# Kernel tuning notes

Measured on AMD Instinct MI355X. Metric: run time of the kernel, lower is better.

The kernel has to match this reference:

```python
import jax, jax.numpy as jnp
import numpy as np

LRELU_SLOPE = 0.2
FUSED_SCALE = float(np.sqrt(2.0))


def _haar_kernels():
    l = np.ones((1, 2), np.float32) / np.sqrt(np.float32(2.0))
    h = l.copy()
    h[0, 0] = -h[0, 0]
    ll = l.T @ l
    lh = h.T @ l
    hl = l.T @ h
    hh = h.T @ h
    return jnp.asarray(ll), jnp.asarray(lh), jnp.asarray(hl), jnp.asarray(hh)


def _blur_kernel():
    k = np.array([1.0, 3.0, 3.0, 1.0], np.float32)
    k = np.outer(k, k)
    k = k / k.sum()
    return jnp.asarray(k)


def upfirdn2d(x, k, up=1, down=1, pad=(0, 0)):
    """Faithful upfirdn2d: zero-upsample by `up`, pad, FIR filter (true
    convolution, i.e. flipped kernel), then stride-`down` decimation.
    Implemented as a single lax conv with lhs_dilation; the extra (up-1)
    trailing pad reproduces torch's H*up zero-padded upsampling."""
    if len(pad) == 2:
        px0, px1, py0, py1 = pad[0], pad[1], pad[0], pad[1]
    else:
        px0, px1, py0, py1 = pad
    B, C, H, W = x.shape
    w = jnp.flip(k, (0, 1))[None, None].astype(x.dtype)  # [1,1,kh,kw]
    out = jax.lax.conv_general_dilated(
        x.reshape(B * C, 1, H, W), w,
        window_strides=(down, down),
        padding=((py0, py1 + up - 1), (px0, px1 + up - 1)),
        lhs_dilation=(up, up),
        dimension_numbers=('NCHW', 'OIHW', 'NCHW'))
    return out.reshape(B, C, out.shape[2], out.shape[3])


def setup_inputs() -> dict:
    key = jax.random.key(0)
    k1, k2 = jax.random.split(key)
    B, C_wt, H, W = 32, 12, 256, 256
    out_channel = 256
    x = jax.random.normal(k1, (B, C_wt, H, W), dtype=jnp.float32)
    weight = jax.random.normal(k2, (out_channel, C_wt, 1, 1), dtype=jnp.float32)
    bias = jnp.zeros((out_channel,), dtype=jnp.float32)
    return {"x": x, "weight": weight, "bias": bias}


def reference(x, weight, bias):
    ll, lh, hl, hh = _haar_kernels()
    c = x.shape[1] // 4
    # InverseHaarTransform (iwt kernels: ll, -lh, -hl, hh), up=2, pad=(1,0,1,0)
    parts = (x[:, 0*c:1*c], x[:, 1*c:2*c], x[:, 2*c:3*c], x[:, 3*c:4*c])
    kerns = (ll, -lh, -hl, hh)
    y = upfirdn2d(parts[0], kerns[0], up=2, pad=(1, 0, 1, 0))
    for p, kk in zip(parts[1:], kerns[1:]):
        y = y + upfirdn2d(p, kk, up=2, pad=(1, 0, 1, 0))
    # Downsample: blur kernel [1,3,3,1], factor=2 -> pad=(1,1), down=2
    y = upfirdn2d(y, _blur_kernel(), down=2, pad=(1, 1))
    # HaarTransform: down=2, pad=(0,0)
    t = jnp.concatenate([upfirdn2d(y, kk, down=2) for kk in (ll, lh, hl, hh)], axis=1)
    # EqualConv2d 1x1 (scale = 1/sqrt(in_channel*k^2), no conv bias) + FusedLeakyReLU
    scale = 1.0 / np.sqrt(np.float32(weight.shape[1]))  # kernel_size = 1
    out = jnp.einsum('bchw,oc->bohw', t, weight[:, :, 0, 0] * scale)
    out = jax.nn.leaky_relu(out + bias[None, :, None, None], LRELU_SLOPE) * FUSED_SCALE
    return t, out
```

## Files before the change

kernel.cpp:

```cpp
#include <hip/hip_runtime.h>


#define T_ELEMS 6291456
#define HW_T    16384
#define HW_X    65536

typedef float f4v __attribute__((ext_vector_type(4)));

__global__ __launch_bounds__(256) void wavelet_t_kernel(
    const float* __restrict__ x, float* __restrict__ t)
{
    const int tid = threadIdx.x;
    const int q   = tid & 31;
    const int ur  = tid >> 5;
    const int u   = blockIdx.x * 8 + ur;
    const int ch  = blockIdx.y;
    const int b   = blockIdx.z;

    const float F[2][2][4] = {
        { { 1.f,  7.f,  7.f,  1.f}, {-1.f, -1.f, 1.f,  1.f} },
        { { 1.f,  5.f, -5.f, -1.f}, {-1.f,  1.f, 1.f, -1.f} }
    };

    float acc[4][4];
    #pragma unroll
    for (int k = 0; k < 4; ++k)
        #pragma unroll
        for (int p = 0; p < 4; ++p) acc[k][p] = 0.f;

    const int r0    = 2 * u - 1;
    const int cbase = 8 * q;

    #pragma unroll
    for (int g = 0; g < 4; ++g) {
        const int gr = g & 1, gc = g >> 1;
        const float* xp = x + ((size_t)(b * 12 + g * 3 + ch)) * HW_X;
        #pragma unroll
        for (int dy = 0; dy < 4; ++dy) {
            const int r = r0 + dy;
            float c[10];
            if (r >= 0 && r < 256) {
                const float* rp = xp + (r << 8) + cbase;
                const float4 A = *reinterpret_cast<const float4*>(rp);
                const float4 B = *reinterpret_cast<const float4*>(rp + 4);
                c[1] = A.x; c[2] = A.y; c[3] = A.z; c[4] = A.w;
                c[5] = B.x; c[6] = B.y; c[7] = B.z; c[8] = B.w;
                float left = 0.f, right = 0.f;
                if (q > 0)  left  = rp[-1];
                if (q < 31) right = rp[8];
                c[0] = left; c[9] = right;
            } else {
                #pragma unroll
                for (int i = 0; i < 10; ++i) c[i] = 0.f;
            }
            #pragma unroll
            for (int p = 0; p < 4; ++p) {
                float s0 = 0.f, s1 = 0.f;
                #pragma unroll
                for (int dx = 0; dx < 4; ++dx) {
                    s0 = fmaf(F[0][gc][dx], c[2 * p + dx], s0);
                    s1 = fmaf(F[1][gc][dx], c[2 * p + dx], s1);
                }
                acc[0][p] = fmaf(F[0][gr][dy], s0, acc[0][p]);
                acc[1][p] = fmaf(F[1][gr][dy], s0, acc[1][p]);
                acc[2][p] = fmaf(F[0][gr][dy], s1, acc[2][p]);
                acc[3][p] = fmaf(F[1][gr][dy], s1, acc[3][p]);
            }
        }
    }

    const float sc = 1.f / 256.f;
    #pragma unroll
    for (int k = 0; k < 4; ++k) {
        float4 o;
        o.x = acc[k][0] * sc; o.y = acc[k][1] * sc;
        o.z = acc[k][2] * sc; o.w = acc[k][3] * sc;
        *reinterpret_cast<float4*>(
            t + ((size_t)(b * 12 + k * 3 + ch)) * HW_T + (u << 7) + 4 * q) = o;
    }
}

__global__ __launch_bounds__(256) void conv1x1_kernel(
    const float* __restrict__ t, const float* __restrict__ w,
    const float* __restrict__ bias, float* __restrict__ out)
{
    __shared__ float ws[128 * 12];
    __shared__ float bs[128];
    const int tid = threadIdx.x;
    const int b   = blockIdx.y;
    const int oz  = blockIdx.z;

    const float scale = 0.2886751345948129f;
    for (int i = tid; i < 1536; i += 256) ws[i] = w[oz * 1536 + i] * scale;
    if (tid < 128) bs[tid] = bias[oz * 128 + tid];
    __syncthreads();

    const int base = blockIdx.x * 1024 + tid * 4;

    float4 tv[12];
    #pragma unroll
    for (int c = 0; c < 12; ++c)
        tv[c] = *reinterpret_cast<const float4*>(t + ((size_t)(b * 12 + c)) * HW_T + base);

    const float SQ2 = 1.4142135623730951f;
    float* outp = out + ((size_t)(b * 256 + oz * 128)) * HW_T + base;

    #pragma unroll 4
    for (int oo = 0; oo < 128; ++oo) {
        const float4 w0 = *reinterpret_cast<const float4*>(&ws[oo * 12 + 0]);
        const float4 w1 = *reinterpret_cast<const float4*>(&ws[oo * 12 + 4]);
        const float4 w2 = *reinterpret_cast<const float4*>(&ws[oo * 12 + 8]);
        const float bo = bs[oo];
        float4 a = make_float4(bo, bo, bo, bo);
        #pragma unroll
        for (int c = 0; c < 4; ++c) {
            const float wv = (&w0.x)[c];
            a.x = fmaf(tv[c].x, wv, a.x); a.y = fmaf(tv[c].y, wv, a.y);
            a.z = fmaf(tv[c].z, wv, a.z); a.w = fmaf(tv[c].w, wv, a.w);
        }
        #pragma unroll
        for (int c = 0; c < 4; ++c) {
            const float wv = (&w1.x)[c];
            a.x = fmaf(tv[c + 4].x, wv, a.x); a.y = fmaf(tv[c + 4].y, wv, a.y);
            a.z = fmaf(tv[c + 4].z, wv, a.z); a.w = fmaf(tv[c + 4].w, wv, a.w);
        }
        #pragma unroll
        for (int c = 0; c < 4; ++c) {
            const float wv = (&w2.x)[c];
            a.x = fmaf(tv[c + 8].x, wv, a.x); a.y = fmaf(tv[c + 8].y, wv, a.y);
            a.z = fmaf(tv[c + 8].z, wv, a.z); a.w = fmaf(tv[c + 8].w, wv, a.w);
        }
        a.x = fmaxf(a.x, 0.2f * a.x) * SQ2;
        a.y = fmaxf(a.y, 0.2f * a.y) * SQ2;
        a.z = fmaxf(a.z, 0.2f * a.z) * SQ2;
        a.w = fmaxf(a.w, 0.2f * a.w) * SQ2;

        f4v av = { a.x, a.y, a.z, a.w };
        __builtin_nontemporal_store(
            av, reinterpret_cast<f4v*>(outp + (size_t)oo * HW_T));
    }
}

extern "C" void kernel_launch(void* const* d_in, const int* in_sizes, int n_in,
                              void* d_out, int out_size, void* d_ws, size_t ws_size,
                              hipStream_t stream) {
    const float* x    = (const float*)d_in[0];
    const float* wgt  = (const float*)d_in[1];
    const float* bias = (const float*)d_in[2];
    float* t   = (float*)d_out;
    float* out = t + T_ELEMS;

    dim3 b1(256, 1, 1), g1(16, 3, 32);
    hipLaunchKernelGGL(wavelet_t_kernel, g1, b1, 0, stream, x, t);

    dim3 b2(256, 1, 1), g2(16, 32, 2);
    hipLaunchKernelGGL(conv1x1_kernel, g2, b2, 0, stream, t, wgt, bias, out);
}
```

Baseline: 153.3 us.

## Fuse wavelet transform and 1x1 conv into a single kernel

```diff
diff --git a/kernel.cpp b/kernel.cpp
--- a/kernel.cpp
+++ b/kernel.cpp
@@ -7,135 +7,131 @@
 
 typedef float f4v __attribute__((ext_vector_type(4)));
 
-__global__ __launch_bounds__(256) void wavelet_t_kernel(
-    const float* __restrict__ x, float* __restrict__ t)
+__global__ __launch_bounds__(256) void fused_fromrgb_kernel(
+    const float* __restrict__ x, const float* __restrict__ w,
+    const float* __restrict__ bias, float* __restrict__ t,
+    float* __restrict__ out)
 {
+    __shared__ float ws[256 * 12];
+    __shared__ float bs[256];
     const int tid = threadIdx.x;
+
+    const float wscale = 0.2886751345948129f;
+    bs[tid] = bias[tid];
+    #pragma unroll
+    for (int i = 0; i < 12; ++i)
+        ws[i * 256 + tid] = w[i * 256 + tid] * wscale;
+
     const int q   = tid & 31;
     const int ur  = tid >> 5;
     const int u   = blockIdx.x * 8 + ur;
-    const int ch  = blockIdx.y;
-    const int b   = blockIdx.z;
+    const int b   = blockIdx.y;
 
     const float F[2][2][4] = {
         { { 1.f,  7.f,  7.f,  1.f}, {-1.f, -1.f, 1.f,  1.f} },
         { { 1.f,  5.f, -5.f, -1.f}, {-1.f,  1.f, 1.f, -1.f} }
     };
 
-    float acc[4][4];
-    #pragma unroll
-    for (int k = 0; k < 4; ++k)
-        #pragma unroll
-        for (int p = 0; p < 4; ++p) acc[k][p] = 0.f;
-
     const int r0    = 2 * u - 1;
     const int cbase = 8 * q;
 
+    float tv[12][4];
+
     #pragma unroll
-    for (int g = 0; g < 4; ++g) {
-        const int gr = g & 1, gc = g >> 1;
-        const float* xp = x + ((size_t)(b * 12 + g * 3 + ch)) * HW_X;
+    for (int ch = 0; ch < 3; ++ch) {
+        float acc[4][4];
         #pragma unroll
-        for (int dy = 0; dy < 4; ++dy) {
-            const int r = r0 + dy;
-            float c[10];
-            if (r >= 0 && r < 256) {
-                const float* rp = xp + (r << 8) + cbase;
-                const float4 A = *reinterpret_cast<const float4*>(rp);
-                const float4 B = *reinterpret_cast<const float4*>(rp + 4);
-                c[1] = A.x; c[2] = A.y; c[3] = A.z; c[4] = A.w;
-                c[5] = B.x; c[6] = B.y; c[7] = B.z; c[8] = B.w;
-                float left = 0.f, right = 0.f;
-                if (q > 0)  left  = rp[-1];
-                if (q < 31) right = rp[8];
-                c[0] = left; c[9] = right;
-            } else {
+        for (int k = 0; k < 4; ++k)
+            #pragma unroll
+            for (int p = 0; p < 4; ++p) acc[k][p] = 0.f;
+
+        #pragma unroll
+        for (int g = 0; g < 4; ++g) {
+            const int gr = g & 1, gc = g >> 1;
+            const float* xp = x + ((size_t)(b * 12 + g * 3 + ch)) * HW_X;
+            #pragma unroll
+            for (int dy = 0; dy < 4; ++dy) {
+                const int r = r0 + dy;
+                float c[10];
+                if (r >= 0 && r < 256) {
+                    const float* rp = xp + (r << 8) + cbase;
+                    const float4 A = *reinterpret_cast<const float4*>(rp);
+                    const float4 B = *reinterpret_cast<const float4*>(rp + 4);
+                    c[1] = A.x; c[2] = A.y; c[3] = A.z; c[4] = A.w;
+                    c[5] = B.x; c[6] = B.y; c[7] = B.z; c[8] = B.w;
+                    float left = 0.f, right = 0.f;
+                    if (q > 0)  left  = rp[-1];
+                    if (q < 31) right = rp[8];
+                    c[0] = left; c[9] = right;
+                } else {
+                    #pragma unroll
+                    for (int i = 0; i < 10; ++i) c[i] = 0.f;
+                }
                 #pragma unroll
-                for (int i = 0; i < 10; ++i) c[i] = 0.f;
+                for (int p = 0; p < 4; ++p) {
+                    float s0 = 0.f, s1 = 0.f;
+                    #pragma unroll
+                    for (int dx = 0; dx < 4; ++dx) {
+                        s0 = fmaf(F[0][gc][dx], c[2 * p + dx], s0);
+                        s1 = fmaf(F[1][gc][dx], c[2 * p + dx], s1);
+                    }
+                    acc[0][p] = fmaf(F[0][gr][dy], s0, acc[0][p]);
+                    acc[1][p] = fmaf(F[1][gr][dy], s0, acc[1][p]);
+                    acc[2][p] = fmaf(F[0][gr][dy], s1, acc[2][p]);
+                    acc[3][p] = fmaf(F[1][gr][dy], s1, acc[3][p]);
+                }
             }
-            #pragma unroll
-            for (int p = 0; p < 4; ++p) {
-                float s0 = 0.f, s1 = 0.f;
-                #pragma unroll
-                for (int dx = 0; dx < 4; ++dx) {
-                    s0 = fmaf(F[0][gc][dx], c[2 * p + dx], s0);
-                    s1 = fmaf(F[1][gc][dx], c[2 * p + dx], s1);
-                }
-                acc[0][p] = fmaf(F[0][gr][dy], s0, acc[0][p]);
-                acc[1][p] = fmaf(F[1][gr][dy], s0, acc[1][p]);
-                acc[2][p] = fmaf(F[0][gr][dy], s1, acc[2][p]);
-                acc[3][p] = fmaf(F[1][gr][dy], s1, acc[3][p]);
-            }
+        }
+
+        const float sc = 1.f / 256.f;
+        #pragma unroll
+        for (int k = 0; k < 4; ++k) {
+            f4v o;
+            o.x = acc[k][0] * sc; o.y = acc[k][1] * sc;
+            o.z = acc[k][2] * sc; o.w = acc[k][3] * sc;
+            tv[k * 3 + ch][0] = o.x; tv[k * 3 + ch][1] = o.y;
+            tv[k * 3 + ch][2] = o.z; tv[k * 3 + ch][3] = o.w;
+            __builtin_nontemporal_store(o, reinterpret_cast<f4v*>(
+                t + ((size_t)(b * 12 + k * 3 + ch)) * HW_T + (u << 7) + 4 * q));
         }
     }
 
-    const float sc = 1.f / 256.f;
-    #pragma unroll
-    for (int k = 0; k < 4; ++k) {
-        float4 o;
-        o.x = acc[k][0] * sc; o.y = acc[k][1] * sc;
-        o.z = acc[k][2] * sc; o.w = acc[k][3] * sc;
-        *reinterpret_cast<float4*>(
-            t + ((size_t)(b * 12 + k * 3 + ch)) * HW_T + (u << 7) + 4 * q) = o;
-    }
-}
-
-__global__ __launch_bounds__(256) void conv1x1_kernel(
-    const float* __restrict__ t, const float* __restrict__ w,
-    const float* __restrict__ bias, float* __restrict__ out)
-{
-    __shared__ float ws[128 * 12];
-    __shared__ float bs[128];
-    const int tid = threadIdx.x;
-    const int b   = blockIdx.y;
-    const int oz  = blockIdx.z;
-
-    const float scale = 0.2886751345948129f;
-    for (int i = tid; i < 1536; i += 256) ws[i] = w[oz * 1536 + i] * scale;
-    if (tid < 128) bs[tid] = bias[oz * 128 + tid];
     __syncthreads();
 
-    const int base = blockIdx.x * 1024 + tid * 4;
+    const float SQ2 = 1.4142135623730951f;
+    const int base = (u << 7) + 4 * q;
+    float* outp = out + ((size_t)b * 256) * HW_T + base;
 
-    float4 tv[12];
-    #pragma unroll
-    for (int c = 0; c < 12; ++c)
-        tv[c] = *reinterpret_cast<const float4*>(t + ((size_t)(b * 12 + c)) * HW_T + base);
-
-    const float SQ2 = 1.4142135623730951f;
-    float* outp = out + ((size_t)(b * 256 + oz * 128)) * HW_T + base;
-
-    #pragma unroll 4
-    for (int oo = 0; oo < 128; ++oo) {
+    #pragma unroll 2
+    for (int oo = 0; oo < 256; ++oo) {
         const float4 w0 = *reinterpret_cast<const float4*>(&ws[oo * 12 + 0]);
         const float4 w1 = *reinterpret_cast<const float4*>(&ws[oo * 12 + 4]);
         const float4 w2 = *reinterpret_cast<const float4*>(&ws[oo * 12 + 8]);
         const float bo = bs[oo];
-        float4 a = make_float4(bo, bo, bo, bo);
+        float a0 = bo, a1 = bo, a2 = bo, a3 = bo;
         #pragma unroll
         for (int c = 0; c < 4; ++c) {
             const float wv = (&w0.x)[c];
-            a.x = fmaf(tv[c].x, wv, a.x); a.y = fmaf(tv[c].y, wv, a.y);
-            a.z = fmaf(tv[c].z, wv, a.z); a.w = fmaf(tv[c].w, wv, a.w);
+            a0 = fmaf(tv[c][0], wv, a0); a1 = fmaf(tv[c][1], wv, a1);
+            a2 = fmaf(tv[c][2], wv, a2); a3 = fmaf(tv[c][3], wv, a3);
         }
         #pragma unroll
         for (int c = 0; c < 4; ++c) {
             const float wv = (&w1.x)[c];
-            a.x = fmaf(tv[c + 4].x, wv, a.x); a.y = fmaf(tv[c + 4].y, wv, a.y);
-            a.z = fmaf(tv[c + 4].z, wv, a.z); a.w = fmaf(tv[c + 4].w, wv, a.w);
+            a0 = fmaf(tv[c + 4][0], wv, a0); a1 = fmaf(tv[c + 4][1], wv, a1);
+            a2 = fmaf(tv[c + 4][2], wv, a2); a3 = fmaf(tv[c + 4][3], wv, a3);
         }
         #pragma unroll
         for (int c = 0; c < 4; ++c) {
             const float wv = (&w2.x)[c];
-            a.x = fmaf(tv[c + 8].x, wv, a.x); a.y = fmaf(tv[c + 8].y, wv, a.y);
-            a.z = fmaf(tv[c + 8].z, wv, a.z); a.w = fmaf(tv[c + 8].w, wv, a.w);
+            a0 = fmaf(tv[c + 8][0], wv, a0); a1 = fmaf(tv[c + 8][1], wv, a1);
+            a2 = fmaf(tv[c + 8][2], wv, a2); a3 = fmaf(tv[c + 8][3], wv, a3);
         }
-        a.x = fmaxf(a.x, 0.2f * a.x) * SQ2;
-        a.y = fmaxf(a.y, 0.2f * a.y) * SQ2;
-        a.z = fmaxf(a.z, 0.2f * a.z) * SQ2;
-        a.w = fmaxf(a.w, 0.2f * a.w) * SQ2;
-
-        f4v av = { a.x, a.y, a.z, a.w };
+        f4v av;
+        av.x = fmaxf(a0, 0.2f * a0) * SQ2;
+        av.y = fmaxf(a1, 0.2f * a1) * SQ2;
+        av.z = fmaxf(a2, 0.2f * a2) * SQ2;
+        av.w = fmaxf(a3, 0.2f * a3) * SQ2;
         __builtin_nontemporal_store(
             av, reinterpret_cast<f4v*>(outp + (size_t)oo * HW_T));
     }
@@ -150,9 +146,7 @@
     float* t   = (float*)d_out;
     float* out = t + T_ELEMS;
 
-    dim3 b1(256, 1, 1), g1(16, 3, 32);
-    hipLaunchKernelGGL(wavelet_t_kernel, g1, b1, 0, stream, x, t);
-
-    dim3 b2(256, 1, 1), g2(16, 32, 2);
-    hipLaunchKernelGGL(conv1x1_kernel, g2, b2, 0, stream, t, wgt, bias, out);
+    dim3 blk(256, 1, 1), grd(16, 32, 1);
+    hipLaunchKernelGGL(fused_fromrgb_kernel, grd, blk, 0, stream,
+                       x, wgt, bias, t, out);
 }
```

Result: faster. 132.7 us (-13.4%).
